# Kernel optimization log

Measured on AMD Instinct MI355X. Metric: run time of the kernel, lower is better.

Reference implementation:

```python
import jax, jax.numpy as jnp
import numpy as np

EPS = 1e-6  # torch.nn.PairwiseDistance default eps, added to the difference


def setup_inputs() -> dict:
    key = jax.random.key(0)
    latents = jax.random.normal(key, (16384, 64, 1, 1), dtype=jnp.float32)
    return {"latents": latents}


def reference(latents) -> jnp.ndarray:
    n = latents.shape[0]
    v = latents.squeeze(-1).squeeze(-1)            # [N, D]
    dp = v @ v.T                                   # [N, N]
    dp = dp.at[jnp.diag_indices(n)].set(-1.0)      # exclude self-match
    idx = jnp.argmax(dp, axis=1)                   # nearest neighbor by dot product
    # PairwiseDistance(p=2): ||x1 - x2 + eps||_2
    dist = jnp.linalg.norm(v - v[idx] + EPS, axis=1)  # [N]
    koleo = -jnp.log(dist * n)
    koleo = jnp.where(koleo < 0, jnp.zeros_like(koleo), koleo)
    return koleo.mean()
```

## Files before the change

kernel.cpp:

```cpp
#include <hip/hip_runtime.h>
#include <math.h>

#define N_PTS 16384
#define DIM   64

typedef short short8 __attribute__((ext_vector_type(8)));
typedef float f32x4  __attribute__((ext_vector_type(4)));

constexpr int TPB     = 512;
constexpr int MI      = 2;
constexpr int CHUNK   = 256;
constexpr int NCH     = N_PTS / CHUNK;
constexpr int NBLK    = NCH * (NCH + 1) / 2;
constexpr int NT      = CHUNK / 16;
constexpr int BSTRIDE = DIM + 8;
constexpr int CSTRIDE = 272;

constexpr float    BIAS    = 2048.0f;
constexpr unsigned KEYMASK = 0xFFFFC000u;

__device__ __forceinline__ unsigned max3u(unsigned a, unsigned b, unsigned c) {
    return max(max(a, b), c);
}

__device__ __forceinline__ short8 pack8(float4 a, float4 b) {
    union { unsigned u[4]; short8 s; } r;
    r.u[0] = __builtin_amdgcn_perm(__float_as_uint(a.y), __float_as_uint(a.x), 0x07060302);
    r.u[1] = __builtin_amdgcn_perm(__float_as_uint(a.w), __float_as_uint(a.z), 0x07060302);
    r.u[2] = __builtin_amdgcn_perm(__float_as_uint(b.y), __float_as_uint(b.x), 0x07060302);
    r.u[3] = __builtin_amdgcn_perm(__float_as_uint(b.w), __float_as_uint(b.z), 0x07060302);
    return r.s;
}

__global__ __launch_bounds__(TPB) void argmax_mfma(const float* __restrict__ vf,
                                                   int* __restrict__ best,
                                                   float* __restrict__ acc,
                                                   unsigned* __restrict__ cnt) {
    __shared__ unsigned short smB[CHUNK * BSTRIDE];
    __shared__ unsigned       colmax4[4 * CSTRIDE];

    const int b = blockIdx.x;
    int ib = (int)((129.0f - sqrtf(16641.0f - 8.0f * (float)b)) * 0.5f);
    while ((64 * (ib + 1) - ((ib + 1) * ib) / 2) <= b) ++ib;
    while ((64 * ib - (ib * (ib - 1)) / 2) > b) --ib;
    const int  jch  = ib + (b - (64 * ib - (ib * (ib - 1)) / 2));
    const bool diag = (ib == jch);
    const int  rb0  = ib  * CHUNK;
    const int  cb0  = jch * CHUNK;

    const int t     = threadIdx.x;
    const int wave  = t >> 6;
    const int lane  = t & 63;
    const int col16 = lane & 15;
    const int quad  = lane >> 4;

    colmax4[t] = 0u;
    if (t < 4 * CSTRIDE - 512) colmax4[512 + t] = 0u;

    if (b == 0 && t == 0) { *acc = 0.0f; *cnt = 0u; }

#pragma unroll
    for (int w = 0; w < 4; ++w) {
        const int s   = t + w * 512;
        const int row = s >> 3;
        const int k8  = s & 7;
        const float4* src = (const float4*)(vf + (size_t)(cb0 + row) * DIM + k8 * 8);
        *(short8*)&smB[row * BSTRIDE + k8 * 8] = pack8(src[0], src[1]);
    }

    const int wave_row0 = rb0 + wave * 32;
    const int loc_row0  = wave * 32;

    short8 a0[MI], a1[MI];
#pragma unroll
    for (int mi = 0; mi < MI; ++mi) {
        const float4* ap = (const float4*)(vf + (size_t)(wave_row0 + mi * 16 + col16) * DIM + quad * 8);
        a0[mi] = pack8(ap[0], ap[1]);
        a1[mi] = pack8(ap[8], ap[9]);
    }

    unsigned bk[MI][4];
#pragma unroll
    for (int mi = 0; mi < MI; ++mi)
#pragma unroll
        for (int r = 0; r < 4; ++r) bk[mi][r] = 0u;

    const f32x4 cinit = {BIAS, BIAS, BIAS, BIAS};

    __syncthreads();

    const unsigned short* bl0 = &smB[col16 * BSTRIDE + quad * 8];
    unsigned* cmbase = &colmax4[quad * CSTRIDE + col16];
    short8 b0 = *(const short8*)(bl0);
    short8 b1 = *(const short8*)(bl0 + 32);

#pragma unroll
    for (int tt = 0; tt < NT; ++tt) {
        const int tn = (tt + 1) & (NT - 1);
        const unsigned short* bln = bl0 + tn * 16 * BSTRIDE;
        short8 nb0 = *(const short8*)(bln);
        short8 nb1 = *(const short8*)(bln + 32);

        f32x4 ac[MI];
#pragma unroll
        for (int mi = 0; mi < MI; ++mi) {
            ac[mi] = __builtin_amdgcn_mfma_f32_16x16x32_bf16(a0[mi], b0, cinit, 0, 0, 0);
            ac[mi] = __builtin_amdgcn_mfma_f32_16x16x32_bf16(a1[mi], b1, ac[mi], 0, 0, 0);
        }

        const int      jb   = cb0 + tt * 16;
        const unsigned jcol = (unsigned)(jb + col16);

#pragma unroll
        for (int mi = 0; mi < MI; ++mi) {
            const int rb = wave_row0 + mi * 16;
            if (diag && rb == jb) {
#pragma unroll
                for (int r = 0; r < 4; ++r) {
                    unsigned key = (__float_as_uint(ac[mi][r]) & KEYMASK) | jcol;
                    if (col16 == quad * 4 + r) key = 0u;
                    bk[mi][r] = max(bk[mi][r], key);
                }
            } else {
#pragma unroll
                for (int r = 0; r < 4; ++r) {
                    unsigned key = (__float_as_uint(ac[mi][r]) & KEYMASK) | jcol;
                    bk[mi][r] = max(bk[mi][r], key);
                }
            }
        }

        if (!diag) {
            unsigned ck[MI * 4];
#pragma unroll
            for (int mi = 0; mi < MI; ++mi)
#pragma unroll
                for (int r = 0; r < 4; ++r)
                    ck[mi * 4 + r] = (__float_as_uint(ac[mi][r]) & KEYMASK)
                                   | (unsigned)(loc_row0 + mi * 16 + quad * 4 + r);
            unsigned mt = max3u(max3u(ck[0], ck[1], ck[2]),
                                max3u(ck[3], ck[4], ck[5]),
                                max(ck[6], ck[7]));
            atomicMax(cmbase + tt * 16, mt);
        }

        b0 = nb0; b1 = nb1;
    }

#pragma unroll
    for (int mi = 0; mi < MI; ++mi) {
#pragma unroll
        for (int r = 0; r < 4; ++r) {
            unsigned k0 = bk[mi][r];
#pragma unroll
            for (int m = 1; m < 16; m <<= 1) {
                unsigned ok = (unsigned)__shfl_xor((int)k0, m);
                k0 = max(k0, ok);
            }
            if (col16 == 0) {
                const int row = wave_row0 + mi * 16 + quad * 4 + r;
                atomicMax(&best[row], (int)k0);
            }
        }
    }

    if (!diag) {
        __syncthreads();
        if (t < CHUNK) {
            const unsigned k = max3u(max(colmax4[t], colmax4[CSTRIDE + t]),
                                     colmax4[2 * CSTRIDE + t],
                                     colmax4[3 * CSTRIDE + t]);
            atomicMax(&best[cb0 + t], (int)(k + (unsigned)rb0));
        }
    }
}

__global__ __launch_bounds__(256) void koleo_kernel(const float* __restrict__ v,
                                                    const int* __restrict__ best,
                                                    float* __restrict__ acc,
                                                    unsigned* __restrict__ cnt,
                                                    float* __restrict__ out) {
    const int i = blockIdx.x * blockDim.x + threadIdx.x;
    const unsigned j = ((unsigned)best[i]) & 0x3FFFu;
    float s = 0.f;
#pragma unroll
    for (int k = 0; k < 16; ++k) {
        float4 a = ((const float4*)(v + (size_t)i * DIM))[k];
        float4 b = ((const float4*)(v + (size_t)j * DIM))[k];
        float dx = a.x - b.x + 1e-6f;
        float dy = a.y - b.y + 1e-6f;
        float dz = a.z - b.z + 1e-6f;
        float dw = a.w - b.w + 1e-6f;
        s += dx * dx + dy * dy + dz * dz + dw * dw;
    }
    float dist = sqrtf(s);
    float kol  = -logf(dist * (float)N_PTS);
    if (kol < 0.f) kol = 0.f;
#pragma unroll
    for (int off = 32; off > 0; off >>= 1) kol += __shfl_down(kol, off);
    if ((threadIdx.x & 63) == 0) atomicAdd(acc, kol);

    __syncthreads();
    if (threadIdx.x == 0) {
        __threadfence();
        unsigned old = atomicAdd(cnt, 1u);
        if (old == gridDim.x - 1) {
            __threadfence();
            float total = atomicAdd(acc, 0.0f);
            out[0] = total / (float)N_PTS;
        }
    }
}

extern "C" void kernel_launch(void* const* d_in, const int* in_sizes, int n_in,
                              void* d_out, int out_size, void* d_ws, size_t ws_size,
                              hipStream_t stream) {
    const float* v   = (const float*)d_in[0];
    float*       out = (float*)d_out;

    int*      best = (int*)d_ws;
    float*    acc  = (float*)((char*)d_ws + (size_t)N_PTS * 4);
    unsigned* cnt  = (unsigned*)(acc + 1);

    argmax_mfma<<<NBLK, TPB, 0, stream>>>(v, best, acc, cnt);
    koleo_kernel<<<N_PTS / 256, 256, 0, stream>>>(v, best, acc, cnt, out);
}
```

Baseline: 99.97 us.

## Compute full dot-product grid instead of exploiting symmetry

Replaces the upper-triangular block schedule, which used symmetry to update both row and column maxima, with a full NCH×NCH grid where each block only updates row maxima. This removes the per-tile LDS atomicMax column reductions, the extra barrier, the shared column buffer and the triangular index math. In exchange it roughly doubles the MFMA work and the B-tile loads.

```diff
diff --git a/kernel.cpp b/kernel.cpp
--- a/kernel.cpp
+++ b/kernel.cpp
@@ -11,17 +11,12 @@
 constexpr int MI      = 2;
 constexpr int CHUNK   = 256;
 constexpr int NCH     = N_PTS / CHUNK;
-constexpr int NBLK    = NCH * (NCH + 1) / 2;
+constexpr int NBLK    = NCH * NCH;
 constexpr int NT      = CHUNK / 16;
 constexpr int BSTRIDE = DIM + 8;
-constexpr int CSTRIDE = 272;
 
 constexpr float    BIAS    = 2048.0f;
 constexpr unsigned KEYMASK = 0xFFFFC000u;
-
-__device__ __forceinline__ unsigned max3u(unsigned a, unsigned b, unsigned c) {
-    return max(max(a, b), c);
-}
 
 __device__ __forceinline__ short8 pack8(float4 a, float4 b) {
     union { unsigned u[4]; short8 s; } r;
@@ -37,13 +32,10 @@
                                                    float* __restrict__ acc,
                                                    unsigned* __restrict__ cnt) {
     __shared__ unsigned short smB[CHUNK * BSTRIDE];
-    __shared__ unsigned       colmax4[4 * CSTRIDE];
 
-    const int b = blockIdx.x;
-    int ib = (int)((129.0f - sqrtf(16641.0f - 8.0f * (float)b)) * 0.5f);
-    while ((64 * (ib + 1) - ((ib + 1) * ib) / 2) <= b) ++ib;
-    while ((64 * ib - (ib * (ib - 1)) / 2) > b) --ib;
-    const int  jch  = ib + (b - (64 * ib - (ib * (ib - 1)) / 2));
+    const int  b    = blockIdx.x;
+    const int  ib   = b >> 6;
+    const int  jch  = b & 63;
     const bool diag = (ib == jch);
     const int  rb0  = ib  * CHUNK;
     const int  cb0  = jch * CHUNK;
@@ -53,9 +45,6 @@
     const int lane  = t & 63;
     const int col16 = lane & 15;
     const int quad  = lane >> 4;
-
-    colmax4[t] = 0u;
-    if (t < 4 * CSTRIDE - 512) colmax4[512 + t] = 0u;
 
     if (b == 0 && t == 0) { *acc = 0.0f; *cnt = 0u; }
 
@@ -69,7 +58,6 @@
     }
 
     const int wave_row0 = rb0 + wave * 32;
-    const int loc_row0  = wave * 32;
 
     short8 a0[MI], a1[MI];
 #pragma unroll
@@ -90,7 +78,6 @@
     __syncthreads();
 
     const unsigned short* bl0 = &smB[col16 * BSTRIDE + quad * 8];
-    unsigned* cmbase = &colmax4[quad * CSTRIDE + col16];
     short8 b0 = *(const short8*)(bl0);
     short8 b1 = *(const short8*)(bl0 + 32);
 
@@ -130,20 +117,6 @@
             }
         }
 
-        if (!diag) {
-            unsigned ck[MI * 4];
-#pragma unroll
-            for (int mi = 0; mi < MI; ++mi)
-#pragma unroll
-                for (int r = 0; r < 4; ++r)
-                    ck[mi * 4 + r] = (__float_as_uint(ac[mi][r]) & KEYMASK)
-                                   | (unsigned)(loc_row0 + mi * 16 + quad * 4 + r);
-            unsigned mt = max3u(max3u(ck[0], ck[1], ck[2]),
-                                max3u(ck[3], ck[4], ck[5]),
-                                max(ck[6], ck[7]));
-            atomicMax(cmbase + tt * 16, mt);
-        }
-
         b0 = nb0; b1 = nb1;
     }
 
@@ -161,16 +134,6 @@
                 const int row = wave_row0 + mi * 16 + quad * 4 + r;
                 atomicMax(&best[row], (int)k0);
             }
-        }
-    }
-
-    if (!diag) {
-        __syncthreads();
-        if (t < CHUNK) {
-            const unsigned k = max3u(max(colmax4[t], colmax4[CSTRIDE + t]),
-                                     colmax4[2 * CSTRIDE + t],
-                                     colmax4[3 * CSTRIDE + t]);
-            atomicMax(&best[cb0 + t], (int)(k + (unsigned)rb0));
         }
     }
 }
```

After: 117.3 us. 1.17x slower.
